# Optimization experiments

Measured on AMD Instinct MI355X. Metric: run time of the kernel, lower is better.

The kernel has to match this reference:

```python
import jax, jax.numpy as jnp
import numpy as np

B, N_HOP, N_MEM, DIM = 1024, 2, 32, 64


def setup_inputs() -> dict:
    key = jax.random.key(0)
    ks = jax.random.split(key, 8)
    # Xavier-ish scales for linear weights
    def xav(k, shape):
        fan_in = shape[-1]
        return jax.random.normal(k, shape, dtype=jnp.float32) * (1.0 / np.sqrt(fan_in))
    return {
        "hs": jax.random.normal(ks[0], (B, N_HOP, N_MEM, DIM), dtype=jnp.float32),
        "Rs": jax.random.normal(ks[1], (B, N_HOP, N_MEM, DIM, DIM), dtype=jnp.float32) * (1.0 / np.sqrt(DIM)),
        "ts": jax.random.normal(ks[2], (B, N_HOP, N_MEM, DIM), dtype=jnp.float32),
        "vs": jax.random.normal(ks[3], (B, DIM), dtype=jnp.float32),
        "W1_w": xav(ks[4], (DIM, 4 * DIM)),
        "W1_b": jnp.zeros((DIM,), dtype=jnp.float32),
        "W2_w": xav(ks[5], (1, DIM)),
        "W2_b": jnp.zeros((1,), dtype=jnp.float32),
        "Wmem_w": xav(ks[6], (N_HOP, DIM, 3 * DIM)),
        "Wmem_b": jnp.zeros((N_HOP, DIM), dtype=jnp.float32),
        "z_w": xav(ks[7], (DIM, 2 * DIM)),
        "z_b": jnp.zeros((DIM,), dtype=jnp.float32),
    }


def reference(hs, Rs, ts, vs, W1_w, W1_b, W2_w, W2_b, Wmem_w, Wmem_b, z_w, z_b):
    """Faithful RippleNetPlus.forward (eval mode: dropout is identity)."""
    M = vs  # prev_mem
    o = vs  # v passed into EpisodicMemory each hop
    n_hop = hs.shape[1]
    for hop in range(n_hop):
        R = Rs[:, hop]   # [B, M, D, D]
        h = hs[:, hop]   # [B, M, D]
        t = ts[:, hop]   # [B, M, D]
        # batched GEMV replacing the B*n_memory Python-loop matmuls
        Rh = jnp.einsum('bmde,bme->bmd', R, h)  # [B, M, D]
        v = o[:, None, :]       # [B, 1, D]
        pm = M[:, None, :]      # [B, 1, D]
        z = jnp.concatenate(
            [Rh * v, Rh * pm, jnp.abs(Rh - v), jnp.abs(Rh - pm)], axis=-1)  # [B, M, 4D]
        hcode = jnp.tanh(jnp.einsum('bmf,df->bmd', z, W1_w) + W1_b)
        Z = (jnp.einsum('bmd,od->bmo', hcode, W2_w) + W2_b)[..., 0]  # [B, M]
        g = jax.nn.softmax(Z, axis=1)[..., None]                     # [B, M, 1]
        o_new = jnp.sum(t * g, axis=1)                               # [B, D]
        concat = jnp.concatenate([M, o_new, o], axis=1)              # [B, 3D]
        M = jax.nn.relu(concat @ Wmem_w[hop].T + Wmem_b[hop])
        o = o_new
    # AnswerModule
    u = jnp.concatenate([M, vs], axis=1) @ z_w.T + z_b  # [B, D]
    return jnp.sum(vs * u, axis=1)  # [B]
```

## Files before the change

### kernel.cpp

```cpp
#include <hip/hip_runtime.h>
#include <math.h>

#define NHOP 2
#define MEM 32
#define DIM 64

typedef __attribute__((ext_vector_type(8))) short short8v;
typedef __attribute__((ext_vector_type(4))) float f32x4;

__device__ __forceinline__ float fast_tanh(float x) {
    const float e = __expf(2.f * x);
    return 1.f - 2.f / (e + 1.f);
}

__device__ __forceinline__ short bf16b(float x) {
    union { float f; unsigned u; } c; c.f = x;
    const unsigned r = c.u + 0x7fffu + ((c.u >> 16) & 1u);
    return (short)(r >> 16);
}

__global__ __launch_bounds__(256, 3) void ripple_fwd(
    const float* __restrict__ hs,
    const float* __restrict__ Rs,
    const float* __restrict__ ts,
    const float* __restrict__ vs,
    const float* __restrict__ W1_w,
    const float* __restrict__ W1_b,
    const float* __restrict__ W2_w,
    const float* __restrict__ W2_b,
    const float* __restrict__ Wmem_w,
    const float* __restrict__ Wmem_b,
    const float* __restrict__ z_w,
    const float* __restrict__ z_b,
    float* __restrict__ out)
{
    __shared__ uint4 W1B[32 * 64];
    __shared__ float Rh_sm[MEM][68];
    __shared__ float M_sm[DIM], o_sm[DIM], onew_sm[DIM], vs_sm[DIM];
    __shared__ float Zp[2][MEM];
    __shared__ float cvec[128];

    const int b   = blockIdx.x;
    const int tid = threadIdx.x;
    const int l   = tid & 63;
    const int wv  = tid >> 6;

    #pragma unroll
    for (int t = 0; t < 8; ++t) {
        const int s    = t * 256 + tid;
        const int frag = s >> 6, ll = s & 63;
        const int kt = frag >> 2, nt = frag & 3;
        const int n  = nt * 16 + (ll & 15);
        const int f0 = kt * 32 + (ll >> 4) * 8;
        const float4 wa = *reinterpret_cast<const float4*>(W1_w + n * 256 + f0);
        const float4 wb = *reinterpret_cast<const float4*>(W1_w + n * 256 + f0 + 4);
        short8v v;
        v[0] = bf16b(wa.x); v[1] = bf16b(wa.y); v[2] = bf16b(wa.z); v[3] = bf16b(wa.w);
        v[4] = bf16b(wb.x); v[5] = bf16b(wb.y); v[6] = bf16b(wb.z); v[7] = bf16b(wb.w);
        *reinterpret_cast<short8v*>(&W1B[s]) = v;
    }
    if (tid < DIM) {
        cvec[tid]      = W1_b[tid];
        cvec[64 + tid] = W2_w[tid];
        const float v = vs[b * DIM + tid];
        M_sm[tid] = v; o_sm[tid] = v; vs_sm[tid] = v;
    }

    const int e0s = l & 3;
    const int dq  = l >> 2;

    for (int hop = 0; hop < NHOP; ++hop) {
        const float* __restrict__ Rbase = Rs + (size_t)(b * NHOP + hop) * MEM * DIM * DIM;
        const float* __restrict__ hbase = hs + (size_t)(b * NHOP + hop) * MEM * DIM;
        const float* __restrict__ tbase = ts + (size_t)(b * NHOP + hop) * MEM * DIM;

        #pragma unroll 2
        for (int k = 0; k < 8; ++k) {
            const int m = k * 4 + wv;
            const float* __restrict__ Rm = Rbase + (size_t)m * DIM * DIM;
            const float* __restrict__ hm = hbase + m * DIM;
            const float4 hv0 = *reinterpret_cast<const float4*>(hm + 4 * e0s);
            const float4 hv1 = *reinterpret_cast<const float4*>(hm + 4 * e0s + 16);
            const float4 hv2 = *reinterpret_cast<const float4*>(hm + 4 * e0s + 32);
            const float4 hv3 = *reinterpret_cast<const float4*>(hm + 4 * e0s + 48);
            #pragma unroll
            for (int dblk = 0; dblk < 4; ++dblk) {
                const int d = dblk * 16 + dq;
                const float* __restrict__ row = Rm + d * DIM + 4 * e0s;
                const float4 r0 = *reinterpret_cast<const float4*>(row);
                const float4 r1 = *reinterpret_cast<const float4*>(row + 16);
                const float4 r2 = *reinterpret_cast<const float4*>(row + 32);
                const float4 r3 = *reinterpret_cast<const float4*>(row + 48);
                float p = r0.x*hv0.x + r0.y*hv0.y + r0.z*hv0.z + r0.w*hv0.w;
                p = fmaf(r1.x, hv1.x, fmaf(r1.y, hv1.y, fmaf(r1.z, hv1.z, fmaf(r1.w, hv1.w, p))));
                p = fmaf(r2.x, hv2.x, fmaf(r2.y, hv2.y, fmaf(r2.z, hv2.z, fmaf(r2.w, hv2.w, p))));
                p = fmaf(r3.x, hv3.x, fmaf(r3.y, hv3.y, fmaf(r3.z, hv3.z, fmaf(r3.w, hv3.w, p))));
                p += __shfl_xor(p, 1);
                p += __shfl_xor(p, 2);
                if (e0s == 0) Rh_sm[m][d] = p;
            }
        }
        __syncthreads();

        {
            const int g   = l >> 4;
            const int col = l & 15;
            const int mt  = wv & 1;
            const int nh  = wv >> 1;
            const int m   = mt * 16 + col;
            f32x4 acc0 = {0.f, 0.f, 0.f, 0.f};
            f32x4 acc1 = {0.f, 0.f, 0.f, 0.f};
            #pragma unroll
            for (int kt = 0; kt < 8; ++kt) {
                const int part = kt >> 1;
                const int e0 = (kt & 1) * 32 + g * 8;
                const float4 r0 = *reinterpret_cast<const float4*>(&Rh_sm[m][e0]);
                const float4 r1 = *reinterpret_cast<const float4*>(&Rh_sm[m][e0 + 4]);
                const float* vsrc = (part & 1) ? M_sm : o_sm;
                const float4 q0 = *reinterpret_cast<const float4*>(vsrc + e0);
                const float4 q1 = *reinterpret_cast<const float4*>(vsrc + e0 + 4);
                float zz[8];
                if (part < 2) {
                    zz[0] = r0.x*q0.x; zz[1] = r0.y*q0.y; zz[2] = r0.z*q0.z; zz[3] = r0.w*q0.w;
                    zz[4] = r1.x*q1.x; zz[5] = r1.y*q1.y; zz[6] = r1.z*q1.z; zz[7] = r1.w*q1.w;
                } else {
                    zz[0] = fabsf(r0.x-q0.x); zz[1] = fabsf(r0.y-q0.y);
                    zz[2] = fabsf(r0.z-q0.z); zz[3] = fabsf(r0.w-q0.w);
                    zz[4] = fabsf(r1.x-q1.x); zz[5] = fabsf(r1.y-q1.y);
                    zz[6] = fabsf(r1.z-q1.z); zz[7] = fabsf(r1.w-q1.w);
                }
                short8v a;
                a[0] = bf16b(zz[0]); a[1] = bf16b(zz[1]); a[2] = bf16b(zz[2]); a[3] = bf16b(zz[3]);
                a[4] = bf16b(zz[4]); a[5] = bf16b(zz[5]); a[6] = bf16b(zz[6]); a[7] = bf16b(zz[7]);
                const short8v b0 = *reinterpret_cast<const short8v*>(&W1B[(kt * 4 + nh * 2 + 0) * 64 + l]);
                const short8v b1 = *reinterpret_cast<const short8v*>(&W1B[(kt * 4 + nh * 2 + 1) * 64 + l]);
                acc0 = __builtin_amdgcn_mfma_f32_16x16x32_bf16(a, b0, acc0, 0, 0, 0);
                acc1 = __builtin_amdgcn_mfma_f32_16x16x32_bf16(a, b1, acc1, 0, 0, 0);
            }
            const int n0 = (nh * 2 + 0) * 16 + col;
            const int n1 = (nh * 2 + 1) * 16 + col;
            const float b1a = cvec[n0], b1b = cvec[n1];
            const float w2a = cvec[64 + n0], w2b = cvec[64 + n1];
            float pz[4];
            #pragma unroll
            for (int r = 0; r < 4; ++r)
                pz[r] = fast_tanh(acc0[r] + b1a) * w2a + fast_tanh(acc1[r] + b1b) * w2b;
            #pragma unroll
            for (int s = 1; s < 16; s <<= 1) {
                pz[0] += __shfl_xor(pz[0], s, 64);
                pz[1] += __shfl_xor(pz[1], s, 64);
                pz[2] += __shfl_xor(pz[2], s, 64);
                pz[3] += __shfl_xor(pz[3], s, 64);
            }
            if (col == 0) {
                #pragma unroll
                for (int r = 0; r < 4; ++r)
                    Zp[nh][mt * 16 + 4 * g + r] = pz[r];
            }
        }
        __syncthreads();

        if (tid < DIM) {
            float mx = -1e30f;
            #pragma unroll
            for (int m = 0; m < MEM; ++m) mx = fmaxf(mx, Zp[0][m] + Zp[1][m]);
            float s = 0.f, accn = 0.f;
            #pragma unroll
            for (int m = 0; m < MEM; ++m) {
                const float e = __expf(Zp[0][m] + Zp[1][m] - mx);
                s += e;
                accn = fmaf(tbase[m * DIM + tid], e, accn);
            }
            const float onew = accn / s;
            onew_sm[tid] = onew;

            const float* __restrict__ Wm = Wmem_w + (size_t)(hop * DIM + tid) * 192;
            float acc2 = Wmem_b[hop * DIM + tid];
            #pragma unroll
            for (int k = 0; k < 16; ++k) {
                const float4 w = *reinterpret_cast<const float4*>(Wm + 4 * k);
                acc2 += w.x * M_sm[4*k] + w.y * M_sm[4*k+1] + w.z * M_sm[4*k+2] + w.w * M_sm[4*k+3];
            }
            #pragma unroll
            for (int k = 0; k < 16; ++k) {
                const float4 w = *reinterpret_cast<const float4*>(Wm + 64 + 4 * k);
                acc2 += w.x * onew_sm[4*k] + w.y * onew_sm[4*k+1] + w.z * onew_sm[4*k+2] + w.w * onew_sm[4*k+3];
            }
            #pragma unroll
            for (int k = 0; k < 16; ++k) {
                const float4 w = *reinterpret_cast<const float4*>(Wm + 128 + 4 * k);
                acc2 += w.x * o_sm[4*k] + w.y * o_sm[4*k+1] + w.z * o_sm[4*k+2] + w.w * o_sm[4*k+3];
            }
            M_sm[tid] = fmaxf(acc2, 0.f);
            o_sm[tid] = onew;
        }
        if (hop == 0) __syncthreads();
    }

    if (tid < DIM) {
        const float* __restrict__ zr = z_w + (size_t)tid * 128;
        float u = z_b[tid];
        #pragma unroll
        for (int k = 0; k < 16; ++k) {
            const float4 w = *reinterpret_cast<const float4*>(zr + 4 * k);
            u += w.x * M_sm[4*k] + w.y * M_sm[4*k+1] + w.z * M_sm[4*k+2] + w.w * M_sm[4*k+3];
        }
        #pragma unroll
        for (int k = 0; k < 16; ++k) {
            const float4 w = *reinterpret_cast<const float4*>(zr + 64 + 4 * k);
            u += w.x * vs_sm[4*k] + w.y * vs_sm[4*k+1] + w.z * vs_sm[4*k+2] + w.w * vs_sm[4*k+3];
        }
        float r = vs_sm[tid] * u;
        #pragma unroll
        for (int s = 1; s < 64; s <<= 1) r += __shfl_xor(r, s, 64);
        if (tid == 0) out[b] = r;
    }
}

extern "C" void kernel_launch(void* const* d_in, const int* in_sizes, int n_in,
                              void* d_out, int out_size, void* d_ws, size_t ws_size,
                              hipStream_t stream)
{
    const float* hs     = (const float*)d_in[0];
    const float* Rs     = (const float*)d_in[1];
    const float* ts     = (const float*)d_in[2];
    const float* vs     = (const float*)d_in[3];
    const float* W1_w   = (const float*)d_in[4];
    const float* W1_b   = (const float*)d_in[5];
    const float* W2_w   = (const float*)d_in[6];
    const float* W2_b   = (const float*)d_in[7];
    const float* Wmem_w = (const float*)d_in[8];
    const float* Wmem_b = (const float*)d_in[9];
    const float* z_w    = (const float*)d_in[10];
    const float* z_b    = (const float*)d_in[11];
    float* out = (float*)d_out;

    const int B = out_size;
    ripple_fwd<<<B, 256, 0, stream>>>(hs, Rs, ts, vs, W1_w, W1_b, W2_w, W2_b,
                                      Wmem_w, Wmem_b, z_w, z_b, out);
}
```

Measured before the change: 215.5 us.

## Split Rh GEMV into separate streaming kernel and keep W1 fragments in registers

```diff
diff --git a/kernel.cpp b/kernel.cpp
--- a/kernel.cpp
+++ b/kernel.cpp
@@ -19,103 +19,124 @@
     return (short)(r >> 16);
 }
 
-__global__ __launch_bounds__(256, 3) void ripple_fwd(
+__global__ __launch_bounds__(256) void rh_stream(
+    const float* __restrict__ Rs,
     const float* __restrict__ hs,
-    const float* __restrict__ Rs,
+    float* __restrict__ rh)
+{
+    const int tid = threadIdx.x;
+    const int l  = tid & 63, wv = tid >> 6;
+    const int e0 = l & 3,  dq = l >> 2;
+    const int mv0 = blockIdx.x * 16 + wv * 4;
+
+    #pragma unroll 2
+    for (int j = 0; j < 4; ++j) {
+        const int idx = mv0 + j;
+        const float* __restrict__ Rm = Rs + (size_t)idx * (DIM * DIM);
+        const float* __restrict__ hm = hs + (size_t)idx * DIM;
+        const float4 hv0 = *reinterpret_cast<const float4*>(hm + 4 * e0);
+        const float4 hv1 = *reinterpret_cast<const float4*>(hm + 4 * e0 + 16);
+        const float4 hv2 = *reinterpret_cast<const float4*>(hm + 4 * e0 + 32);
+        const float4 hv3 = *reinterpret_cast<const float4*>(hm + 4 * e0 + 48);
+        float p[4];
+        #pragma unroll
+        for (int dblk = 0; dblk < 4; ++dblk) {
+            const int d = 4 * dq + dblk;
+            const float* __restrict__ row = Rm + d * DIM + 4 * e0;
+            const float4 r0 = *reinterpret_cast<const float4*>(row);
+            const float4 r1 = *reinterpret_cast<const float4*>(row + 16);
+            const float4 r2 = *reinterpret_cast<const float4*>(row + 32);
+            const float4 r3 = *reinterpret_cast<const float4*>(row + 48);
+            float s = r0.x*hv0.x + r0.y*hv0.y + r0.z*hv0.z + r0.w*hv0.w;
+            s = fmaf(r1.x, hv1.x, fmaf(r1.y, hv1.y, fmaf(r1.z, hv1.z, fmaf(r1.w, hv1.w, s))));
+            s = fmaf(r2.x, hv2.x, fmaf(r2.y, hv2.y, fmaf(r2.z, hv2.z, fmaf(r2.w, hv2.w, s))));
+            s = fmaf(r3.x, hv3.x, fmaf(r3.y, hv3.y, fmaf(r3.z, hv3.z, fmaf(r3.w, hv3.w, s))));
+            s += __shfl_xor(s, 1);
+            s += __shfl_xor(s, 2);
+            p[dblk] = s;
+        }
+        if (e0 == 0) {
+            const float4 v = make_float4(p[0], p[1], p[2], p[3]);
+            *reinterpret_cast<float4*>(rh + (size_t)idx * DIM + 4 * dq) = v;
+        }
+    }
+}
+
+__global__ __launch_bounds__(256) void ripple_chain(
+    const float* __restrict__ rh,
     const float* __restrict__ ts,
     const float* __restrict__ vs,
     const float* __restrict__ W1_w,
     const float* __restrict__ W1_b,
     const float* __restrict__ W2_w,
-    const float* __restrict__ W2_b,
     const float* __restrict__ Wmem_w,
     const float* __restrict__ Wmem_b,
     const float* __restrict__ z_w,
     const float* __restrict__ z_b,
     float* __restrict__ out)
 {
-    __shared__ uint4 W1B[32 * 64];
-    __shared__ float Rh_sm[MEM][68];
+    __shared__ float Rh_sm[NHOP][MEM][68];
     __shared__ float M_sm[DIM], o_sm[DIM], onew_sm[DIM], vs_sm[DIM];
     __shared__ float Zp[2][MEM];
-    __shared__ float cvec[128];
 
     const int b   = blockIdx.x;
     const int tid = threadIdx.x;
     const int l   = tid & 63;
     const int wv  = tid >> 6;
 
-    #pragma unroll
-    for (int t = 0; t < 8; ++t) {
-        const int s    = t * 256 + tid;
-        const int frag = s >> 6, ll = s & 63;
-        const int kt = frag >> 2, nt = frag & 3;
-        const int n  = nt * 16 + (ll & 15);
-        const int f0 = kt * 32 + (ll >> 4) * 8;
-        const float4 wa = *reinterpret_cast<const float4*>(W1_w + n * 256 + f0);
-        const float4 wb = *reinterpret_cast<const float4*>(W1_w + n * 256 + f0 + 4);
-        short8v v;
-        v[0] = bf16b(wa.x); v[1] = bf16b(wa.y); v[2] = bf16b(wa.z); v[3] = bf16b(wa.w);
-        v[4] = bf16b(wb.x); v[5] = bf16b(wb.y); v[6] = bf16b(wb.z); v[7] = bf16b(wb.w);
-        *reinterpret_cast<short8v*>(&W1B[s]) = v;
+    {
+        const float* __restrict__ src = rh + (size_t)b * (NHOP * MEM * DIM);
+        #pragma unroll
+        for (int it = 0; it < 4; ++it) {
+            const int s   = it * 1024 + tid * 4;
+            const int row = s >> 6, col = s & 63;
+            *reinterpret_cast<float4*>(&Rh_sm[0][0][0] + row * 68 + col) =
+                *reinterpret_cast<const float4*>(src + s);
+        }
     }
     if (tid < DIM) {
-        cvec[tid]      = W1_b[tid];
-        cvec[64 + tid] = W2_w[tid];
         const float v = vs[b * DIM + tid];
         M_sm[tid] = v; o_sm[tid] = v; vs_sm[tid] = v;
     }
 
-    const int e0s = l & 3;
-    const int dq  = l >> 2;
+    const int g   = l >> 4;
+    const int col = l & 15;
+    const int mt  = wv & 1;
+    const int nh  = wv >> 1;
+    short8v wfrag[8][2];
+    #pragma unroll
+    for (int kt = 0; kt < 8; ++kt) {
+        #pragma unroll
+        for (int q = 0; q < 2; ++q) {
+            const int n  = (nh * 2 + q) * 16 + col;
+            const int f0 = kt * 32 + g * 8;
+            const float4 wa = *reinterpret_cast<const float4*>(W1_w + n * 256 + f0);
+            const float4 wb = *reinterpret_cast<const float4*>(W1_w + n * 256 + f0 + 4);
+            short8v v;
+            v[0] = bf16b(wa.x); v[1] = bf16b(wa.y); v[2] = bf16b(wa.z); v[3] = bf16b(wa.w);
+            v[4] = bf16b(wb.x); v[5] = bf16b(wb.y); v[6] = bf16b(wb.z); v[7] = bf16b(wb.w);
+            wfrag[kt][q] = v;
+        }
+    }
+    const int n0 = (nh * 2 + 0) * 16 + col;
+    const int n1 = (nh * 2 + 1) * 16 + col;
+    const float b1a = W1_b[n0], b1b = W1_b[n1];
+    const float w2a = W2_w[n0], w2b = W2_w[n1];
+    __syncthreads();
 
     for (int hop = 0; hop < NHOP; ++hop) {
-        const float* __restrict__ Rbase = Rs + (size_t)(b * NHOP + hop) * MEM * DIM * DIM;
-        const float* __restrict__ hbase = hs + (size_t)(b * NHOP + hop) * MEM * DIM;
         const float* __restrict__ tbase = ts + (size_t)(b * NHOP + hop) * MEM * DIM;
 
-        #pragma unroll 2
-        for (int k = 0; k < 8; ++k) {
-            const int m = k * 4 + wv;
-            const float* __restrict__ Rm = Rbase + (size_t)m * DIM * DIM;
-            const float* __restrict__ hm = hbase + m * DIM;
-            const float4 hv0 = *reinterpret_cast<const float4*>(hm + 4 * e0s);
-            const float4 hv1 = *reinterpret_cast<const float4*>(hm + 4 * e0s + 16);
-            const float4 hv2 = *reinterpret_cast<const float4*>(hm + 4 * e0s + 32);
-            const float4 hv3 = *reinterpret_cast<const float4*>(hm + 4 * e0s + 48);
-            #pragma unroll
-            for (int dblk = 0; dblk < 4; ++dblk) {
-                const int d = dblk * 16 + dq;
-                const float* __restrict__ row = Rm + d * DIM + 4 * e0s;
-                const float4 r0 = *reinterpret_cast<const float4*>(row);
-                const float4 r1 = *reinterpret_cast<const float4*>(row + 16);
-                const float4 r2 = *reinterpret_cast<const float4*>(row + 32);
-                const float4 r3 = *reinterpret_cast<const float4*>(row + 48);
-                float p = r0.x*hv0.x + r0.y*hv0.y + r0.z*hv0.z + r0.w*hv0.w;
-                p = fmaf(r1.x, hv1.x, fmaf(r1.y, hv1.y, fmaf(r1.z, hv1.z, fmaf(r1.w, hv1.w, p))));
-                p = fmaf(r2.x, hv2.x, fmaf(r2.y, hv2.y, fmaf(r2.z, hv2.z, fmaf(r2.w, hv2.w, p))));
-                p = fmaf(r3.x, hv3.x, fmaf(r3.y, hv3.y, fmaf(r3.z, hv3.z, fmaf(r3.w, hv3.w, p))));
-                p += __shfl_xor(p, 1);
-                p += __shfl_xor(p, 2);
-                if (e0s == 0) Rh_sm[m][d] = p;
-            }
-        }
-        __syncthreads();
-
         {
-            const int g   = l >> 4;
-            const int col = l & 15;
-            const int mt  = wv & 1;
-            const int nh  = wv >> 1;
-            const int m   = mt * 16 + col;
+            const int m = mt * 16 + col;
             f32x4 acc0 = {0.f, 0.f, 0.f, 0.f};
             f32x4 acc1 = {0.f, 0.f, 0.f, 0.f};
             #pragma unroll
             for (int kt = 0; kt < 8; ++kt) {
                 const int part = kt >> 1;
                 const int e0 = (kt & 1) * 32 + g * 8;
-                const float4 r0 = *reinterpret_cast<const float4*>(&Rh_sm[m][e0]);
-                const float4 r1 = *reinterpret_cast<const float4*>(&Rh_sm[m][e0 + 4]);
+                const float4 r0 = *reinterpret_cast<const float4*>(&Rh_sm[hop][m][e0]);
+                const float4 r1 = *reinterpret_cast<const float4*>(&Rh_sm[hop][m][e0 + 4]);
                 const float* vsrc = (part & 1) ? M_sm : o_sm;
                 const float4 q0 = *reinterpret_cast<const float4*>(vsrc + e0);
                 const float4 q1 = *reinterpret_cast<const float4*>(vsrc + e0 + 4);
@@ -132,15 +153,9 @@
                 short8v a;
                 a[0] = bf16b(zz[0]); a[1] = bf16b(zz[1]); a[2] = bf16b(zz[2]); a[3] = bf16b(zz[3]);
                 a[4] = bf16b(zz[4]); a[5] = bf16b(zz[5]); a[6] = bf16b(zz[6]); a[7] = bf16b(zz[7]);
-                const short8v b0 = *reinterpret_cast<const short8v*>(&W1B[(kt * 4 + nh * 2 + 0) * 64 + l]);
-                const short8v b1 = *reinterpret_cast<const short8v*>(&W1B[(kt * 4 + nh * 2 + 1) * 64 + l]);
-                acc0 = __builtin_amdgcn_mfma_f32_16x16x32_bf16(a, b0, acc0, 0, 0, 0);
-                acc1 = __builtin_amdgcn_mfma_f32_16x16x32_bf16(a, b1, acc1, 0, 0, 0);
-            }
-            const int n0 = (nh * 2 + 0) * 16 + col;
-            const int n1 = (nh * 2 + 1) * 16 + col;
-            const float b1a = cvec[n0], b1b = cvec[n1];
-            const float w2a = cvec[64 + n0], w2b = cvec[64 + n1];
+                acc0 = __builtin_amdgcn_mfma_f32_16x16x32_bf16(a, wfrag[kt][0], acc0, 0, 0, 0);
+                acc1 = __builtin_amdgcn_mfma_f32_16x16x32_bf16(a, wfrag[kt][1], acc1, 0, 0, 0);
+            }
             float pz[4];
             #pragma unroll
             for (int r = 0; r < 4; ++r)
@@ -194,7 +209,7 @@
             M_sm[tid] = fmaxf(acc2, 0.f);
             o_sm[tid] = onew;
         }
-        if (hop == 0) __syncthreads();
+        __syncthreads();
     }
 
     if (tid < DIM) {
@@ -228,14 +243,17 @@
     const float* W1_w   = (const float*)d_in[4];
     const float* W1_b   = (const float*)d_in[5];
     const float* W2_w   = (const float*)d_in[6];
-    const float* W2_b   = (const float*)d_in[7];
     const float* Wmem_w = (const float*)d_in[8];
     const float* Wmem_b = (const float*)d_in[9];
     const float* z_w    = (const float*)d_in[10];
     const float* z_b    = (const float*)d_in[11];
     float* out = (float*)d_out;
+    float* rh  = (float*)d_ws;
 
     const int B = out_size;
-    ripple_fwd<<<B, 256, 0, stream>>>(hs, Rs, ts, vs, W1_w, W1_b, W2_w, W2_b,
-                                      Wmem_w, Wmem_b, z_w, z_b, out);
-}
+    const int gridA = B * NHOP * MEM / 16;
+    rh_stream<<<gridA, 256, 0, stream>>>(Rs, hs, rh);
+    ripple_chain<<<B, 256, 0, stream>>>(rh, ts, vs, W1_w, W1_b, (const float*)d_in[6],
+                                        Wmem_w, Wmem_b, z_w, z_b, out);
+    (void)W1_w; (void)ws_size; (void)n_in; (void)in_sizes;
+}
```

Result: slower. 246.8 us (+14.5%).
